# Optimization experiments

Hardware: AMD Instinct MI355X
Metric: run time of the kernel (lower is better)

## Reference

```python
import jax, jax.numpy as jnp
import numpy as np
import math

DIM_IN = 2
DIM_HIDDEN = 64
DIM_OUT = 16
NUM_LAYERS = 5  # num_layers-1 = 4 hidden SirenLayers per subnet + 1 last layer
W0 = 30.0
W0_INITIAL = 30.0
S0 = 0.0
C = 6.0
N_POINTS = 262144


def wire(w0, s0, z):
    # sin(w0*z) * exp(-(s0*z)^2)
    return jnp.sin(w0 * z) * jnp.exp(-jnp.square(s0 * z))


def setup_inputs() -> dict:
    key = jax.random.key(0)
    ks = jax.random.split(key, 8)
    # NOTE: source passes is_first=False for every layer, so init bound is
    # sqrt(c/dim_in)/layer_w0 for ALL layers (including the first).
    std0 = math.sqrt(C / DIM_IN) / W0_INITIAL
    stdh = math.sqrt(C / DIM_HIDDEN) / W0
    stdl = math.sqrt(C / DIM_HIDDEN) / W0
    u = lambda k, shape, s: jax.random.uniform(k, shape, jnp.float32, -s, s)
    nmid = NUM_LAYERS - 2  # hidden->hidden layers per subnet (3)
    return {
        "x": jax.random.uniform(ks[0], (N_POINTS, DIM_IN), jnp.float32),
        "W0m": u(ks[1], (DIM_OUT, DIM_HIDDEN, DIM_IN), std0),
        "b0": u(ks[2], (DIM_OUT, DIM_HIDDEN), std0),
        "Wm": u(ks[3], (nmid, DIM_OUT, DIM_HIDDEN, DIM_HIDDEN), stdh),
        "bm": u(ks[4], (nmid, DIM_OUT, DIM_HIDDEN), stdh),
        "Wl": u(ks[5], (DIM_OUT, DIM_HIDDEN), stdl),
        "bl": u(ks[6], (DIM_OUT,), stdl),
    }


def reference(x, W0m, b0, Wm, bm, Wl, bl):
    # First layer of each subnet (uses w0_initial): [N,D] x [O,H,D] -> [N,O,H]
    h = wire(W0_INITIAL, S0, jnp.einsum("nd,ohd->noh", x, W0m) + b0)
    # Middle hidden layers (w0), scanned over the fixed layer stack.
    def body(h, wb):
        W, b = wb
        h = wire(W0, S0, jnp.einsum("noh,ogh->nog", h, W) + b)
        return h, None
    h, _ = jax.lax.scan(body, h, (Wm, bm))
    # Last layer per subnet: dim 1 output each, is_last -> +0.5, no activation.
    out = jnp.einsum("noh,oh->no", h, Wl) + bl + 0.5  # [N, dim_out]
    return out
```

## Files before the change

kernel.cpp:

```cpp
#include <hip/hip_runtime.h>

typedef short bf16x8 __attribute__((ext_vector_type(8)));
typedef float f32x16 __attribute__((ext_vector_type(16)));
typedef float f32x2  __attribute__((ext_vector_type(2)));

#define NBGROUPS 128
#define SCALE 4.7746482927568601f

union Frag { bf16x8 v; unsigned u[4]; uint4 q; };

__device__ __forceinline__ unsigned pk_bf16(float lo, float hi) {
    unsigned r;
    asm("v_cvt_pk_bf16_f32 %0, %1, %2" : "=v"(r) : "v"(lo), "v"(hi));
    return r;
}
__device__ __forceinline__ float lo_f(unsigned w) { return __uint_as_float(w << 16); }
__device__ __forceinline__ float hi_f(unsigned w) { return __uint_as_float(w & 0xffff0000u); }

__device__ __forceinline__ f32x2 sin2(f32x2 z) {
    f32x2 r  = { rintf(z.x), rintf(z.y) };
    f32x2 v  = z - r;
    f32x2 v2 = v * v;
    f32x2 p  = { 32.765379f, 32.765379f };
    p = __builtin_elementwise_fma(p, v2, (f32x2){-74.468884f, -74.468884f});
    p = __builtin_elementwise_fma(p, v2, (f32x2){ 81.365064f,  81.365064f});
    p = __builtin_elementwise_fma(p, v2, (f32x2){-41.331084f, -41.331084f});
    p = __builtin_elementwise_fma(p, v2, (f32x2){  6.2830526f,  6.2830526f});
    return p * v;
}

struct BiasRegs { f32x2 p[2][8]; };
__device__ __forceinline__ BiasRegs load_bias(const float4* ldsBias, int Lb, int hi) {
    BiasRegs br;
#pragma unroll
    for (int tg = 0; tg < 2; ++tg) {
        const float4* base = &ldsBias[((Lb*2+tg)*2 + hi)*4];
#pragma unroll
        for (int q = 0; q < 4; ++q) {
            float4 b = base[q];
            br.p[tg][2*q]   = (f32x2){b.x, b.y};
            br.p[tg][2*q+1] = (f32x2){b.z, b.w};
        }
    }
    return br;
}

__device__ __forceinline__ void transitionHL(const f32x16* acc, const BiasRegs& br,
                                             Frag* Bhi, Frag* Blo) {
#pragma unroll
    for (int tg = 0; tg < 2; ++tg)
#pragma unroll
        for (int j = 0; j < 8; ++j) {
            f32x2 z = (f32x2){ acc[tg][2*j], acc[tg][2*j+1] } + br.p[tg][j];
            f32x2 s = sin2(z);
            unsigned ph = pk_bf16(s.x, s.y);
            f32x2 hf = { lo_f(ph), hi_f(ph) };
            f32x2 d  = s - hf;
            Bhi[tg*2 + (j>>2)].u[j&3] = ph;
            Blo[tg*2 + (j>>2)].u[j&3] = pk_bf16(d.x, d.y);
        }
}
__device__ __forceinline__ void transitionH(const f32x16* acc, const BiasRegs& br, Frag* Bhi) {
#pragma unroll
    for (int tg = 0; tg < 2; ++tg)
#pragma unroll
        for (int j = 0; j < 8; ++j) {
            f32x2 z = (f32x2){ acc[tg][2*j], acc[tg][2*j+1] } + br.p[tg][j];
            f32x2 s = sin2(z);
            Bhi[tg*2 + (j>>2)].u[j&3] = pk_bf16(s.x, s.y);
        }
}

__global__ __launch_bounds__(256, 2)
void siren_kernel(const float* __restrict__ x, const float* __restrict__ W0m,
                  const float* __restrict__ b0, const float* __restrict__ Wm,
                  const float* __restrict__ bm, const float* __restrict__ Wl,
                  const float* __restrict__ bl, float* __restrict__ out)
{
    __shared__ uint4  ldsAhi[3*2*4*64];
    __shared__ uint4  ldsAlo[2*2*4*64];
    __shared__ float4 ldsBias[4*2*2*4];
    __shared__ float  ldsWl[2][32];

    const int tid  = threadIdx.x;
    const int o    = blockIdx.x;
    const int pg   = blockIdx.y;
    const int lane = tid & 63;
    const int wv   = tid >> 6;
    const int col  = lane & 31;
    const int hi   = lane >> 5;

    for (int idx = tid; idx < 3*2*4*64; idx += 256) {
        int l2  = idx & 63;
        int fi  = idx >> 6;
        int c   = fi & 3;
        int tg  = (fi >> 2) & 1;
        int L   = fi >> 3;
        int hi2 = l2 >> 5;
        int g   = tg*32 + (l2 & 31);
        int th  = c >> 1, s = c & 1;
        const float2* Wrow2 = (const float2*)(Wm + (((size_t)(L*16 + o)*64 + g)*64));
        uint4 whi, wlo;
        unsigned* uh = (unsigned*)&whi;
        unsigned* ul = (unsigned*)&wlo;
#pragma unroll
        for (int wi = 0; wi < 4; ++wi) {
            int h = th*32 + s*16 + 8*(wi>>1) + 2*(wi&1) + 4*hi2;
            float2 wp = Wrow2[h >> 1];
            float a = SCALE*wp.x, b = SCALE*wp.y;
            unsigned ph = pk_bf16(a, b);
            uh[wi] = ph;
            ul[wi] = pk_bf16(a - lo_f(ph), b - hi_f(ph));
        }
        ldsAhi[idx] = whi;
        if (idx < 2*2*4*64) ldsAlo[idx] = wlo;
    }
    if (tid < 64) {
        int q   = tid & 3;
        int hi2 = (tid >> 2) & 1;
        int tg  = (tid >> 3) & 1;
        int Lb  = tid >> 4;
        int h0  = tg*32 + 8*q + 4*hi2;
        const float* bsrc = (Lb < 3) ? (bm + (Lb*16 + o)*64) : (b0 + o*64);
        ldsBias[tid] = make_float4(SCALE*bsrc[h0], SCALE*bsrc[h0+1],
                                   SCALE*bsrc[h0+2], SCALE*bsrc[h0+3]);
    }
    if (tid >= 64 && tid < 128) {
        int t2  = tid - 64;
        int hi2 = t2 >> 5;
        int idx = t2 & 31;
        int tg  = idx >> 4;
        int r   = idx & 15;
        int s = r >> 3, j = r & 7;
        int h = tg*32 + 16*s + (j & 3) + 8*(j >> 2) + 4*hi2;
        ldsWl[hi2][idx] = Wl[o*64 + h];
    }

    Frag L1A[2];
#pragma unroll
    for (int tg = 0; tg < 2; ++tg) {
        int g = tg*32 + col;
        float2 wp = ((const float2*)W0m)[o*64 + g];
        float s0 = SCALE*wp.x, s1 = SCALE*wp.y;
        unsigned u0 = pk_bf16(s0, s0), u1 = pk_bf16(s1, s1);
        float l0 = s0 - lo_f(u0), l1 = s1 - lo_f(u1);
        L1A[tg].u[0] = hi ? 0u : u0;
        L1A[tg].u[1] = hi ? 0u : u1;
        L1A[tg].u[2] = hi ? 0u : pk_bf16(l0, l0);
        L1A[tg].u[3] = hi ? 0u : pk_bf16(l1, l1);
    }
    const float blv = bl[o] + 0.5f;

    f32x16 zero16;
#pragma unroll
    for (int i = 0; i < 16; ++i) zero16[i] = 0.f;

    __syncthreads();

    const int tbase = pg*64 + wv;
#pragma unroll 1
    for (int k = 0; k < 8; ++k) {
        const int ta  = tbase + 8*k;
        const int ppa = ta*32 + col;
        const int ppb = ppa + 128;

        float2 xa = ((const float2*)x)[ppa];
        float2 xb = ((const float2*)x)[ppb];
        Frag B1a, B1b;
        {
            unsigned ux = pk_bf16(xa.x, xa.y);
            float x0h = lo_f(ux), x1h = hi_f(ux);
            unsigned w0 = pk_bf16(x0h, xa.x - x0h);
            unsigned w1 = pk_bf16(x1h, xa.y - x1h);
            B1a.u[0] = hi ? 0u : w0;  B1a.u[1] = hi ? 0u : w1;
            B1a.u[2] = hi ? 0u : w0;  B1a.u[3] = hi ? 0u : w1;
            ux = pk_bf16(xb.x, xb.y);
            x0h = lo_f(ux); x1h = hi_f(ux);
            w0 = pk_bf16(x0h, xb.x - x0h);
            w1 = pk_bf16(x1h, xb.y - x1h);
            B1b.u[0] = hi ? 0u : w0;  B1b.u[1] = hi ? 0u : w1;
            B1b.u[2] = hi ? 0u : w0;  B1b.u[3] = hi ? 0u : w1;
        }

        BiasRegs br3 = load_bias(ldsBias, 3, hi);
        f32x16 accA[2], accB[2];
        accA[0] = __builtin_amdgcn_mfma_f32_32x32x16_bf16(L1A[0].v, B1a.v, zero16, 0, 0, 0);
        accA[1] = __builtin_amdgcn_mfma_f32_32x32x16_bf16(L1A[1].v, B1a.v, zero16, 0, 0, 0);
        accB[0] = __builtin_amdgcn_mfma_f32_32x32x16_bf16(L1A[0].v, B1b.v, zero16, 0, 0, 0);
        accB[1] = __builtin_amdgcn_mfma_f32_32x32x16_bf16(L1A[1].v, B1b.v, zero16, 0, 0, 0);

        Frag BhiA[4], BloA[4], BhiB[4], BloB[4];
        transitionHL(accA, br3, BhiA, BloA);
        transitionHL(accB, br3, BhiB, BloB);

#pragma unroll
        for (int L = 0; L < 2; ++L) {
            BiasRegs br = load_bias(ldsBias, L, hi);
#pragma unroll
            for (int c = 0; c < 4; ++c) {
                Frag Ah0, Ah1, Al0, Al1;
                Ah0.q = ldsAhi[((L*2+0)*4+c)*64 + lane];
                Ah1.q = ldsAhi[((L*2+1)*4+c)*64 + lane];
                Al0.q = ldsAlo[((L*2+0)*4+c)*64 + lane];
                Al1.q = ldsAlo[((L*2+1)*4+c)*64 + lane];
                accA[0] = __builtin_amdgcn_mfma_f32_32x32x16_bf16(Ah0.v, BhiA[c].v, (c==0)?zero16:accA[0], 0, 0, 0);
                accA[1] = __builtin_amdgcn_mfma_f32_32x32x16_bf16(Ah1.v, BhiA[c].v, (c==0)?zero16:accA[1], 0, 0, 0);
                accB[0] = __builtin_amdgcn_mfma_f32_32x32x16_bf16(Ah0.v, BhiB[c].v, (c==0)?zero16:accB[0], 0, 0, 0);
                accB[1] = __builtin_amdgcn_mfma_f32_32x32x16_bf16(Ah1.v, BhiB[c].v, (c==0)?zero16:accB[1], 0, 0, 0);
                accA[0] = __builtin_amdgcn_mfma_f32_32x32x16_bf16(Ah0.v, BloA[c].v, accA[0], 0, 0, 0);
                accA[1] = __builtin_amdgcn_mfma_f32_32x32x16_bf16(Ah1.v, BloA[c].v, accA[1], 0, 0, 0);
                accB[0] = __builtin_amdgcn_mfma_f32_32x32x16_bf16(Ah0.v, BloB[c].v, accB[0], 0, 0, 0);
                accB[1] = __builtin_amdgcn_mfma_f32_32x32x16_bf16(Ah1.v, BloB[c].v, accB[1], 0, 0, 0);
                accA[0] = __builtin_amdgcn_mfma_f32_32x32x16_bf16(Al0.v, BhiA[c].v, accA[0], 0, 0, 0);
                accA[1] = __builtin_amdgcn_mfma_f32_32x32x16_bf16(Al1.v, BhiA[c].v, accA[1], 0, 0, 0);
                accB[0] = __builtin_amdgcn_mfma_f32_32x32x16_bf16(Al0.v, BhiB[c].v, accB[0], 0, 0, 0);
                accB[1] = __builtin_amdgcn_mfma_f32_32x32x16_bf16(Al1.v, BhiB[c].v, accB[1], 0, 0, 0);
            }
            if (L == 0) {
                transitionHL(accA, br, BhiA, BloA);
                transitionHL(accB, br, BhiB, BloB);
            } else {
                transitionH(accA, br, BhiA);
                transitionH(accB, br, BhiB);
            }
        }

#pragma unroll
        for (int c = 0; c < 4; ++c) {
            Frag Ah0, Ah1;
            Ah0.q = ldsAhi[((2*2+0)*4+c)*64 + lane];
            Ah1.q = ldsAhi[((2*2+1)*4+c)*64 + lane];
            accA[0] = __builtin_amdgcn_mfma_f32_32x32x16_bf16(Ah0.v, BhiA[c].v, (c==0)?zero16:accA[0], 0, 0, 0);
            accA[1] = __builtin_amdgcn_mfma_f32_32x32x16_bf16(Ah1.v, BhiA[c].v, (c==0)?zero16:accA[1], 0, 0, 0);
            accB[0] = __builtin_amdgcn_mfma_f32_32x32x16_bf16(Ah0.v, BhiB[c].v, (c==0)?zero16:accB[0], 0, 0, 0);
            accB[1] = __builtin_amdgcn_mfma_f32_32x32x16_bf16(Ah1.v, BhiB[c].v, (c==0)?zero16:accB[1], 0, 0, 0);
        }

        BiasRegs br2 = load_bias(ldsBias, 2, hi);
        const f32x2* wl2 = (const f32x2*)&ldsWl[hi][0];
        f32x2 sa = {0.f, 0.f}, sb = {0.f, 0.f};
#pragma unroll
        for (int tg = 0; tg < 2; ++tg)
#pragma unroll
            for (int j = 0; j < 8; ++j) {
                f32x2 w = wl2[tg*8 + j];
                f32x2 za = (f32x2){ accA[tg][2*j], accA[tg][2*j+1] } + br2.p[tg][j];
                f32x2 zb = (f32x2){ accB[tg][2*j], accB[tg][2*j+1] } + br2.p[tg][j];
                sa = __builtin_elementwise_fma(sin2(za), w, sa);
                sb = __builtin_elementwise_fma(sin2(zb), w, sb);
            }
        float suma = sa.x + sa.y;
        float sumb = sb.x + sb.y;
        suma += __shfl_xor(suma, 32);
        sumb += __shfl_xor(sumb, 32);
        if (lane < 32) {
            out[(size_t)ppa*16 + o] = suma + blv;
            out[(size_t)ppb*16 + o] = sumb + blv;
        }
    }
}

extern "C" void kernel_launch(void* const* d_in, const int* in_sizes, int n_in,
                              void* d_out, int out_size, void* d_ws, size_t ws_size,
                              hipStream_t stream) {
    (void)in_sizes; (void)n_in; (void)out_size; (void)d_ws; (void)ws_size;
    siren_kernel<<<dim3(16, NBGROUPS), dim3(256), 0, stream>>>(
        (const float*)d_in[0], (const float*)d_in[1], (const float*)d_in[2],
        (const float*)d_in[3], (const float*)d_in[4], (const float*)d_in[5],
        (const float*)d_in[6], (float*)d_out);
}
```

Measured before the change: 360.3 us.

## Interleave per-tile layer MFMAs with sine transitions and raise MFMA priority

The hidden-layer loop is restructured so tile A's MFMA chain for a layer is issued right after its sine transition, while tile B's transition runs, and then the roles swap. This lets matrix-core work on one point tile overlap with VALU sine work on the other. MFMA blocks are wrapped in s_setprio(1)/s_setprio(0) so waves issuing matrix work are favoured. The grid is also transposed so consecutive blocks share the same subnet o, which changes how weight loads hit the cache and how work lands on CUs.

```diff
diff --git a/kernel.cpp b/kernel.cpp
--- a/kernel.cpp
+++ b/kernel.cpp
@@ -71,6 +71,41 @@
         }
 }
 
+__device__ __forceinline__ void layerHL(f32x16* acc, const Frag* Bhi, const Frag* Blo,
+                                        const uint4* ldsAhi, const uint4* ldsAlo,
+                                        int L, int lane, const f32x16& zero16) {
+    __builtin_amdgcn_s_setprio(1);
+#pragma unroll
+    for (int c = 0; c < 4; ++c) {
+        Frag Ah0, Ah1, Al0, Al1;
+        Ah0.q = ldsAhi[((L*2+0)*4+c)*64 + lane];
+        Ah1.q = ldsAhi[((L*2+1)*4+c)*64 + lane];
+        Al0.q = ldsAlo[((L*2+0)*4+c)*64 + lane];
+        Al1.q = ldsAlo[((L*2+1)*4+c)*64 + lane];
+        acc[0] = __builtin_amdgcn_mfma_f32_32x32x16_bf16(Ah0.v, Bhi[c].v, (c==0)?zero16:acc[0], 0, 0, 0);
+        acc[1] = __builtin_amdgcn_mfma_f32_32x32x16_bf16(Ah1.v, Bhi[c].v, (c==0)?zero16:acc[1], 0, 0, 0);
+        acc[0] = __builtin_amdgcn_mfma_f32_32x32x16_bf16(Ah0.v, Blo[c].v, acc[0], 0, 0, 0);
+        acc[1] = __builtin_amdgcn_mfma_f32_32x32x16_bf16(Ah1.v, Blo[c].v, acc[1], 0, 0, 0);
+        acc[0] = __builtin_amdgcn_mfma_f32_32x32x16_bf16(Al0.v, Bhi[c].v, acc[0], 0, 0, 0);
+        acc[1] = __builtin_amdgcn_mfma_f32_32x32x16_bf16(Al1.v, Bhi[c].v, acc[1], 0, 0, 0);
+    }
+    __builtin_amdgcn_s_setprio(0);
+}
+__device__ __forceinline__ void layerH(f32x16* acc, const Frag* Bhi,
+                                       const uint4* ldsAhi, int L, int lane,
+                                       const f32x16& zero16) {
+    __builtin_amdgcn_s_setprio(1);
+#pragma unroll
+    for (int c = 0; c < 4; ++c) {
+        Frag Ah0, Ah1;
+        Ah0.q = ldsAhi[((L*2+0)*4+c)*64 + lane];
+        Ah1.q = ldsAhi[((L*2+1)*4+c)*64 + lane];
+        acc[0] = __builtin_amdgcn_mfma_f32_32x32x16_bf16(Ah0.v, Bhi[c].v, (c==0)?zero16:acc[0], 0, 0, 0);
+        acc[1] = __builtin_amdgcn_mfma_f32_32x32x16_bf16(Ah1.v, Bhi[c].v, (c==0)?zero16:acc[1], 0, 0, 0);
+    }
+    __builtin_amdgcn_s_setprio(0);
+}
+
 __global__ __launch_bounds__(256, 2)
 void siren_kernel(const float* __restrict__ x, const float* __restrict__ W0m,
                   const float* __restrict__ b0, const float* __restrict__ Wm,
@@ -83,8 +118,8 @@
     __shared__ float  ldsWl[2][32];
 
     const int tid  = threadIdx.x;
-    const int o    = blockIdx.x;
-    const int pg   = blockIdx.y;
+    const int pg   = blockIdx.x;
+    const int o    = blockIdx.y;
     const int lane = tid & 63;
     const int wv   = tid >> 6;
     const int col  = lane & 31;
@@ -184,57 +219,29 @@
 
         BiasRegs br3 = load_bias(ldsBias, 3, hi);
         f32x16 accA[2], accB[2];
+
+        __builtin_amdgcn_s_setprio(1);
         accA[0] = __builtin_amdgcn_mfma_f32_32x32x16_bf16(L1A[0].v, B1a.v, zero16, 0, 0, 0);
         accA[1] = __builtin_amdgcn_mfma_f32_32x32x16_bf16(L1A[1].v, B1a.v, zero16, 0, 0, 0);
         accB[0] = __builtin_amdgcn_mfma_f32_32x32x16_bf16(L1A[0].v, B1b.v, zero16, 0, 0, 0);
         accB[1] = __builtin_amdgcn_mfma_f32_32x32x16_bf16(L1A[1].v, B1b.v, zero16, 0, 0, 0);
+        __builtin_amdgcn_s_setprio(0);
 
         Frag BhiA[4], BloA[4], BhiB[4], BloB[4];
         transitionHL(accA, br3, BhiA, BloA);
+        layerHL(accA, BhiA, BloA, ldsAhi, ldsAlo, 0, lane, zero16);
         transitionHL(accB, br3, BhiB, BloB);
-
-#pragma unroll
-        for (int L = 0; L < 2; ++L) {
-            BiasRegs br = load_bias(ldsBias, L, hi);
-#pragma unroll
-            for (int c = 0; c < 4; ++c) {
-                Frag Ah0, Ah1, Al0, Al1;
-                Ah0.q = ldsAhi[((L*2+0)*4+c)*64 + lane];
-                Ah1.q = ldsAhi[((L*2+1)*4+c)*64 + lane];
-                Al0.q = ldsAlo[((L*2+0)*4+c)*64 + lane];
-                Al1.q = ldsAlo[((L*2+1)*4+c)*64 + lane];
-                accA[0] = __builtin_amdgcn_mfma_f32_32x32x16_bf16(Ah0.v, BhiA[c].v, (c==0)?zero16:accA[0], 0, 0, 0);
-                accA[1] = __builtin_amdgcn_mfma_f32_32x32x16_bf16(Ah1.v, BhiA[c].v, (c==0)?zero16:accA[1], 0, 0, 0);
-                accB[0] = __builtin_amdgcn_mfma_f32_32x32x16_bf16(Ah0.v, BhiB[c].v, (c==0)?zero16:accB[0], 0, 0, 0);
-                accB[1] = __builtin_amdgcn_mfma_f32_32x32x16_bf16(Ah1.v, BhiB[c].v, (c==0)?zero16:accB[1], 0, 0, 0);
-                accA[0] = __builtin_amdgcn_mfma_f32_32x32x16_bf16(Ah0.v, BloA[c].v, accA[0], 0, 0, 0);
-                accA[1] = __builtin_amdgcn_mfma_f32_32x32x16_bf16(Ah1.v, BloA[c].v, accA[1], 0, 0, 0);
-                accB[0] = __builtin_amdgcn_mfma_f32_32x32x16_bf16(Ah0.v, BloB[c].v, accB[0], 0, 0, 0);
-                accB[1] = __builtin_amdgcn_mfma_f32_32x32x16_bf16(Ah1.v, BloB[c].v, accB[1], 0, 0, 0);
-                accA[0] = __builtin_amdgcn_mfma_f32_32x32x16_bf16(Al0.v, BhiA[c].v, accA[0], 0, 0, 0);
-                accA[1] = __builtin_amdgcn_mfma_f32_32x32x16_bf16(Al1.v, BhiA[c].v, accA[1], 0, 0, 0);
-                accB[0] = __builtin_amdgcn_mfma_f32_32x32x16_bf16(Al0.v, BhiB[c].v, accB[0], 0, 0, 0);
-                accB[1] = __builtin_amdgcn_mfma_f32_32x32x16_bf16(Al1.v, BhiB[c].v, accB[1], 0, 0, 0);
-            }
-            if (L == 0) {
-                transitionHL(accA, br, BhiA, BloA);
-                transitionHL(accB, br, BhiB, BloB);
-            } else {
-                transitionH(accA, br, BhiA);
-                transitionH(accB, br, BhiB);
-            }
-        }
-
-#pragma unroll
-        for (int c = 0; c < 4; ++c) {
-            Frag Ah0, Ah1;
-            Ah0.q = ldsAhi[((2*2+0)*4+c)*64 + lane];
-            Ah1.q = ldsAhi[((2*2+1)*4+c)*64 + lane];
-            accA[0] = __builtin_amdgcn_mfma_f32_32x32x16_bf16(Ah0.v, BhiA[c].v, (c==0)?zero16:accA[0], 0, 0, 0);
-            accA[1] = __builtin_amdgcn_mfma_f32_32x32x16_bf16(Ah1.v, BhiA[c].v, (c==0)?zero16:accA[1], 0, 0, 0);
-            accB[0] = __builtin_amdgcn_mfma_f32_32x32x16_bf16(Ah0.v, BhiB[c].v, (c==0)?zero16:accB[0], 0, 0, 0);
-            accB[1] = __builtin_amdgcn_mfma_f32_32x32x16_bf16(Ah1.v, BhiB[c].v, (c==0)?zero16:accB[1], 0, 0, 0);
-        }
+        layerHL(accB, BhiB, BloB, ldsAhi, ldsAlo, 0, lane, zero16);
+        BiasRegs br0 = load_bias(ldsBias, 0, hi);
+        transitionHL(accA, br0, BhiA, BloA);
+        layerHL(accA, BhiA, BloA, ldsAhi, ldsAlo, 1, lane, zero16);
+        transitionHL(accB, br0, BhiB, BloB);
+        layerHL(accB, BhiB, BloB, ldsAhi, ldsAlo, 1, lane, zero16);
+        BiasRegs br1 = load_bias(ldsBias, 1, hi);
+        transitionH(accA, br1, BhiA);
+        layerH(accA, BhiA, ldsAhi, 2, lane, zero16);
+        transitionH(accB, br1, BhiB);
+        layerH(accB, BhiB, ldsAhi, 2, lane, zero16);
 
         BiasRegs br2 = load_bias(ldsBias, 2, hi);
         const f32x2* wl2 = (const f32x2*)&ldsWl[hi][0];
@@ -264,7 +271,7 @@
                               void* d_out, int out_size, void* d_ws, size_t ws_size,
                               hipStream_t stream) {
     (void)in_sizes; (void)n_in; (void)out_size; (void)d_ws; (void)ws_size;
-    siren_kernel<<<dim3(16, NBGROUPS), dim3(256), 0, stream>>>(
+    siren_kernel<<<dim3(NBGROUPS, 16), dim3(256), 0, stream>>>(
         (const float*)d_in[0], (const float*)d_in[1], (const float*)d_in[2],
         (const float*)d_in[3], (const float*)d_in[4], (const float*)d_in[5],
         (const float*)d_in[6], (float*)d_out);
```

After: 369.2 us. 2.4% more time.
